# Kernel optimization log

Measured on AMD Instinct MI355X. Metric: run time of the kernel, lower is better.

The kernel has to match this reference:

```python
import jax, jax.numpy as jnp
import numpy as np

B, S, D, C = 4, 4096, 2048, 64  # batch, seq, d_model, num_channels (sqrt(4096)=64)
TEMP = 1.0
LN_EPS = 1e-5
AGG_EPS = 1e-8


def _layer_norm(x, g, b):
    m = x.mean(-1, keepdims=True)
    v = ((x - m) ** 2).mean(-1, keepdims=True)
    return (x - m) / jnp.sqrt(v + LN_EPS) * g + b


def setup_inputs() -> dict:
    key = jax.random.key(0)
    ks = jax.random.split(key, 8)
    s = 1.0 / np.sqrt(D)
    return {
        "x": jax.random.normal(ks[0], (B, S, D), jnp.float32),
        "attention_mask": jnp.ones((B, S), jnp.float32),
        "ln_gamma": jnp.ones((D,), jnp.float32),
        "ln_beta": jnp.zeros((D,), jnp.float32),
        "Wq": jax.random.normal(ks[1], (D, D), jnp.float32) * s,
        "Wk": jax.random.normal(ks[2], (D, D), jnp.float32) * s,
        "Wv": jax.random.normal(ks[3], (D, D), jnp.float32) * s,
        "Wr": jax.random.normal(ks[4], (C, D), jnp.float32) * s,
        "br": jnp.zeros((C,), jnp.float32),
        "Wa": jax.random.normal(ks[5], (D, D), jnp.float32) * s,
        "ba": jnp.zeros((D,), jnp.float32),
        "Wout": jax.random.normal(ks[6], (D, D), jnp.float32) * s,
        "bout": jnp.zeros((D,), jnp.float32),
    }


def reference(x, attention_mask, ln_gamma, ln_beta, Wq, Wk, Wv, Wr, br, Wa, ba, Wout, bout):
    residual = x
    h = _layer_norm(x, ln_gamma, ln_beta)
    q = h @ Wq.T  # [B,S,D]
    k = h @ Wk.T
    v = h @ Wv.T
    m = attention_mask[..., None]
    q = q * m
    k = k * m
    v = v * m

    # --- dynamic router: logits -> softmax, top-1 channel id + gathered weight ---
    routing_input = q + 0.1 * k
    probs = jax.nn.softmax((routing_input @ Wr.T + br) / TEMP, axis=-1)  # [B,S,C]
    channel_ids = jnp.argmax(probs, axis=-1)  # [B,S] int
    w = jnp.take_along_axis(probs, channel_ids[..., None], axis=-1)  # [B,S,1] top-1 weight

    # --- learnable channel aggregator: scatter-reduce tokens -> channels ---
    onehot = jax.nn.one_hot(channel_ids, C, dtype=v.dtype)  # [B,S,C]
    dispatch = onehot * w  # weighted dispatch mask
    ch_sum = jnp.einsum('bsc,bsd->bcd', dispatch, v)  # [B,C,D]
    ch_den = dispatch.sum(axis=1)  # [B,C]
    ch_mean = ch_sum / (ch_den[..., None] + AGG_EPS)
    ch_out = ch_mean @ Wa.T + ba  # learnable channel transform [B,C,D]
    # gather channel summary back to each token, weighted by routing weight
    aggregated = jnp.einsum('bsc,bcd->bsd', onehot, ch_out) * w  # [B,S,D]

    # --- regularization term ---
    q_norm = jnp.linalg.norm(q, axis=-1, keepdims=True)
    k_norm = jnp.linalg.norm(k, axis=-1, keepdims=True)
    reg = 0.001 * (q_norm + k_norm).mean()

    output = aggregated @ Wout.T + bout
    output = output + reg  # broadcast scalar reg_term
    output = output + residual
    return output
```

## Files before the change

### kernel.cpp

```cpp
#include <hip/hip_runtime.h>
#include <hip/hip_bf16.h>

typedef unsigned short u16;
typedef __bf16 bf16x8 __attribute__((ext_vector_type(8)));
typedef float  f32x4  __attribute__((ext_vector_type(4)));

#define B_   4
#define S_   4096
#define D_   2048
#define C_   64
#define T_   (B_*S_)
#define NALL 6144
#define NCH  16

__device__ __forceinline__ u16 f2bf(float f) {
  union { float f; unsigned u; } c; c.f = f;
  unsigned r = c.u + 0x7FFFu + ((c.u >> 16) & 1u);
  return (u16)(r >> 16);
}
__device__ __forceinline__ float bf2f(u16 u) {
  union { float f; unsigned u; } c; c.u = ((unsigned)u) << 16;
  return c.f;
}

__device__ __forceinline__ void gload16(const u16* g, u16* l) {
  __builtin_amdgcn_global_load_lds(
      (__attribute__((address_space(1))) void*)(void*)g,
      (__attribute__((address_space(3))) void*)l, 16, 0, 0);
}

template<int EPI>
__global__ __launch_bounds__(256)
void gemm_bt(const u16* __restrict__ A, const u16* __restrict__ BT, int K,
             const float* __restrict__ mask,
             float* __restrict__ qn2, float* __restrict__ kn2,
             u16* __restrict__ uout, float* __restrict__ fout,
             const float* __restrict__ bias)
{
  __shared__ u16 lA[128 * 32];
  __shared__ u16 lB[128 * 32];
  const int bm = blockIdx.x, bn = blockIdx.y;
  const int tid = threadIdx.x;
  const int wid = tid >> 6, lane = tid & 63;
  const int wm = wid >> 1, wn = wid & 1;
  const int lcol = lane & 15, khalf = lane >> 4;
  const int kb = khalf * 8;

  f32x4 acc[4][4] = {};

  const u16* Ab = A + (size_t)bm * 128 * K;
  const u16* Bb = BT + (size_t)bn * 128 * K;
  const int arow = wm * 64 + lcol;
  const int brow = wn * 64 + lcol;

  for (int kt = 0; kt < K; kt += 32) {
#pragma unroll
    for (int i = 0; i < 2; ++i) {
      int idx = tid + i * 256;
      int r = idx >> 2, ko = (idx & 3) << 3;
      gload16(Ab + (size_t)r * K + kt + ko, &lA[idx * 8]);
      gload16(Bb + (size_t)r * K + kt + ko, &lB[idx * 8]);
    }
    __syncthreads();
    bf16x8 av[4], bv[4];
#pragma unroll
    for (int f = 0; f < 4; ++f) {
      av[f] = *(const bf16x8*)&lA[(arow + f * 16) * 32 + kb];
      bv[f] = *(const bf16x8*)&lB[(brow + f * 16) * 32 + kb];
    }
#pragma unroll
    for (int m = 0; m < 4; ++m)
#pragma unroll
      for (int n = 0; n < 4; ++n)
        acc[m][n] = __builtin_amdgcn_mfma_f32_16x16x32_bf16(av[m], bv[n], acc[m][n], 0, 0, 0);
    __syncthreads();
  }

  const int r0 = bm * 128 + wm * 64;
  const int c0 = bn * 128 + wn * 64;
  const int lrow = khalf * 4;

  if constexpr (EPI == 0) {
    const int region = bn >> 4;
#pragma unroll
    for (int fm = 0; fm < 4; ++fm) {
#pragma unroll
      for (int i = 0; i < 4; ++i) {
        int row = r0 + fm * 16 + lrow + i;
        float mv = mask[row];
        if (region < 2) {
          float ss = 0.f;
#pragma unroll
          for (int fn = 0; fn < 4; ++fn) { float v = acc[fm][fn][i] * mv; ss += v * v; }
#pragma unroll
          for (int d = 1; d < 16; d <<= 1) ss += __shfl_xor(ss, d);
          if (lcol == 0) atomicAdd((region == 0 ? qn2 : kn2) + row, ss);
        } else {
#pragma unroll
          for (int fn = 0; fn < 4; ++fn) {
            int col = c0 + fn * 16 + lcol - 4096;
            uout[(size_t)row * D_ + col] = f2bf(acc[fm][fn][i] * mv);
          }
        }
      }
    }
  } else if constexpr (EPI == 2) {
#pragma unroll
    for (int fm = 0; fm < 4; ++fm)
#pragma unroll
      for (int i = 0; i < 4; ++i) {
        int row = r0 + fm * 16 + lrow + i;
#pragma unroll
        for (int fn = 0; fn < 4; ++fn) {
          int col = c0 + fn * 16 + lcol;
          uout[(size_t)row * D_ + col] = f2bf(acc[fm][fn][i] + bias[col]);
        }
      }
  } else {
#pragma unroll
    for (int fm = 0; fm < 4; ++fm)
#pragma unroll
      for (int i = 0; i < 4; ++i) {
        int row = r0 + fm * 16 + lrow + i;
#pragma unroll
        for (int fn = 0; fn < 4; ++fn) {
          int col = c0 + fn * 16 + lcol;
          fout[(size_t)row * D_ + col] = acc[fm][fn][i];
        }
      }
  }
}

__global__ __launch_bounds__(256)
void gemm4_bt(const u16* __restrict__ Ah, const u16* __restrict__ Al,
              const u16* __restrict__ Bh, const u16* __restrict__ Bl,
              int K, int rlim, float* __restrict__ out, int ldo)
{
  __shared__ u16 lAh[128 * 32];
  __shared__ u16 lAl[128 * 32];
  __shared__ u16 lBh[64 * 32];
  __shared__ u16 lBl[64 * 32];
  const int bm = blockIdx.x, bn = blockIdx.y;
  const int tid = threadIdx.x;
  const int wid = tid >> 6, lane = tid & 63;
  const int lcol = lane & 15, khalf = lane >> 4;
  const int kb = khalf * 8;

  f32x4 acc[2][4] = {};

  const u16* Abh = Ah + (size_t)bm * 128 * K;
  const u16* Abl = Al + (size_t)bm * 128 * K;
  const u16* Bbh = Bh + (size_t)bn * 64 * K;
  const u16* Bbl = Bl + (size_t)bn * 64 * K;
  const int arow = wid * 32 + lcol;

  for (int kt = 0; kt < K; kt += 32) {
#pragma unroll
    for (int i = 0; i < 2; ++i) {
      int idx = tid + i * 256;
      int r = idx >> 2, ko = (idx & 3) << 3;
      gload16(Abh + (size_t)r * K + kt + ko, &lAh[idx * 8]);
      gload16(Abl + (size_t)r * K + kt + ko, &lAl[idx * 8]);
    }
    {
      int r = tid >> 2, ko = (tid & 3) << 3;
      gload16(Bbh + (size_t)r * K + kt + ko, &lBh[tid * 8]);
      gload16(Bbl + (size_t)r * K + kt + ko, &lBl[tid * 8]);
    }
    __syncthreads();
    bf16x8 ah[2], al[2], bh[4], bl[4];
#pragma unroll
    for (int f = 0; f < 2; ++f) {
      ah[f] = *(const bf16x8*)&lAh[(arow + f * 16) * 32 + kb];
      al[f] = *(const bf16x8*)&lAl[(arow + f * 16) * 32 + kb];
    }
#pragma unroll
    for (int f = 0; f < 4; ++f) {
      bh[f] = *(const bf16x8*)&lBh[(f * 16 + lcol) * 32 + kb];
      bl[f] = *(const bf16x8*)&lBl[(f * 16 + lcol) * 32 + kb];
    }
#pragma unroll
    for (int m = 0; m < 2; ++m)
#pragma unroll
      for (int n = 0; n < 4; ++n) {
        acc[m][n] = __builtin_amdgcn_mfma_f32_16x16x32_bf16(ah[m], bh[n], acc[m][n], 0, 0, 0);
        acc[m][n] = __builtin_amdgcn_mfma_f32_16x16x32_bf16(ah[m], bl[n], acc[m][n], 0, 0, 0);
        acc[m][n] = __builtin_amdgcn_mfma_f32_16x16x32_bf16(al[m], bh[n], acc[m][n], 0, 0, 0);
        acc[m][n] = __builtin_amdgcn_mfma_f32_16x16x32_bf16(al[m], bl[n], acc[m][n], 0, 0, 0);
      }
    __syncthreads();
  }

  const int r0 = bm * 128 + wid * 32;
#pragma unroll
  for (int fm = 0; fm < 2; ++fm)
#pragma unroll
    for (int i = 0; i < 4; ++i) {
      int row = r0 + fm * 16 + khalf * 4 + i;
      if (row < rlim) {
#pragma unroll
        for (int fn = 0; fn < 4; ++fn) {
          int col = bn * 64 + fn * 16 + lcol;
          out[(size_t)row * ldo + col] = acc[fm][fn][i];
        }
      }
    }
}

__global__ __launch_bounds__(256)
void ln_kernel(const float* __restrict__ x, const float* __restrict__ g,
               const float* __restrict__ be, u16* __restrict__ h, u16* __restrict__ hl)
{
  const int row = blockIdx.x, tid = threadIdx.x;
  const int wid = tid >> 6, lane = tid & 63;
  const float* xr = x + (size_t)row * D_;
  float4 a = *(const float4*)(xr + tid * 4);
  float4 b = *(const float4*)(xr + 1024 + tid * 4);
  float s = a.x + a.y + a.z + a.w + b.x + b.y + b.z + b.w;
  float q = a.x * a.x + a.y * a.y + a.z * a.z + a.w * a.w +
            b.x * b.x + b.y * b.y + b.z * b.z + b.w * b.w;
#pragma unroll
  for (int d = 1; d < 64; d <<= 1) { s += __shfl_xor(s, d); q += __shfl_xor(q, d); }
  __shared__ float ls[4], lq[4];
  if (lane == 0) { ls[wid] = s; lq[wid] = q; }
  __syncthreads();
  s = ls[0] + ls[1] + ls[2] + ls[3];
  q = lq[0] + lq[1] + lq[2] + lq[3];
  const float mean = s * (1.0f / D_);
  const float var = q * (1.0f / D_) - mean * mean;
  const float rstd = rsqrtf(var + 1e-5f);

#pragma unroll
  for (int half = 0; half < 2; ++half) {
    int base = half * 1024 + tid * 4;
    float4 xv = half ? b : a;
    float4 gv = *(const float4*)(g + base);
    float4 bv = *(const float4*)(be + base);
    float v0 = (xv.x - mean) * rstd * gv.x + bv.x;
    float v1 = (xv.y - mean) * rstd * gv.y + bv.y;
    float v2 = (xv.z - mean) * rstd * gv.z + bv.z;
    float v3 = (xv.w - mean) * rstd * gv.w + bv.w;
    ushort4 oh, ol;
    oh.x = f2bf(v0); ol.x = f2bf(v0 - bf2f(oh.x));
    oh.y = f2bf(v1); ol.y = f2bf(v1 - bf2f(oh.y));
    oh.z = f2bf(v2); ol.z = f2bf(v2 - bf2f(oh.z));
    oh.w = f2bf(v3); ol.w = f2bf(v3 - bf2f(oh.w));
    *(ushort4*)(h  + (size_t)row * D_ + base) = oh;
    *(ushort4*)(hl + (size_t)row * D_ + base) = ol;
  }
}

__global__ __launch_bounds__(256)
void castf2b(const float* __restrict__ in, u16* __restrict__ out, int n)
{
  int i = (blockIdx.x * 256 + threadIdx.x) * 4;
  if (i >= n) return;
  float4 v = *(const float4*)(in + i);
  ushort4 o; o.x = f2bf(v.x); o.y = f2bf(v.y); o.z = f2bf(v.z); o.w = f2bf(v.w);
  *(ushort4*)(out + i) = o;
}

__global__ __launch_bounds__(256)
void splitf(const float* __restrict__ in, u16* __restrict__ hi, u16* __restrict__ lo, int n)
{
  int i = (blockIdx.x * 256 + threadIdx.x) * 4;
  if (i >= n) return;
  float4 v = *(const float4*)(in + i);
  ushort4 h, l;
  h.x = f2bf(v.x); l.x = f2bf(v.x - bf2f(h.x));
  h.y = f2bf(v.y); l.y = f2bf(v.y - bf2f(h.y));
  h.z = f2bf(v.z); l.z = f2bf(v.z - bf2f(h.z));
  h.w = f2bf(v.w); l.w = f2bf(v.w - bf2f(h.w));
  *(ushort4*)(hi + i) = h;
  *(ushort4*)(lo + i) = l;
}

__global__ __launch_bounds__(256)
void wqk_t(const float* __restrict__ Wq, const float* __restrict__ Wk,
           u16* __restrict__ Th, u16* __restrict__ Tl)
{
  __shared__ float t[32][33];
  const int bx = blockIdx.x * 32, by = blockIdx.y * 32;
  const int tx = threadIdx.x & 31, ty = threadIdx.x >> 5;
#pragma unroll
  for (int j = 0; j < 32; j += 8) {
    int aa = by + ty + j, ee = bx + tx;
    t[ty + j][tx] = Wq[(size_t)aa * D_ + ee] + 0.1f * Wk[(size_t)aa * D_ + ee];
  }
  __syncthreads();
#pragma unroll
  for (int j = 0; j < 32; j += 8) {
    int ee = bx + ty + j, aa = by + tx;
    float v = t[tx][ty + j];
    u16 h = f2bf(v);
    Th[(size_t)ee * D_ + aa] = h;
    Tl[(size_t)ee * D_ + aa] = f2bf(v - bf2f(h));
  }
}

__global__ __launch_bounds__(256)
void reg_reduce(const float* __restrict__ qn2, const float* __restrict__ kn2,
                float* __restrict__ racc)
{
  int i = blockIdx.x * 256 + threadIdx.x;
  int lane = threadIdx.x & 63, wid = threadIdx.x >> 6;
  float v = sqrtf(qn2[i]) + sqrtf(kn2[i]);
#pragma unroll
  for (int d = 1; d < 64; d <<= 1) v += __shfl_xor(v, d);
  __shared__ float lsum[4];
  if (lane == 0) lsum[wid] = v;
  __syncthreads();
  if (threadIdx.x == 0) atomicAdd(racc, lsum[0] + lsum[1] + lsum[2] + lsum[3]);
}

__global__ __launch_bounds__(256)
void router_kernel(const float* __restrict__ logits, const float* __restrict__ br,
                   int* __restrict__ cid, float* __restrict__ wt, float* __restrict__ chden)
{
  const int tid = threadIdx.x, wid = tid >> 6, lane = tid & 63;
  const int t = blockIdx.x * 4 + wid;
  float l = logits[(size_t)t * C_ + lane] + br[lane];
  float mx = l;
#pragma unroll
  for (int d = 1; d < 64; d <<= 1) mx = fmaxf(mx, __shfl_xor(mx, d));
  float e = __expf(l - mx);
  float s = e;
#pragma unroll
  for (int d = 1; d < 64; d <<= 1) s += __shfl_xor(s, d);
  unsigned long long ball = __ballot(l == mx);
  if (lane == 0) {
    int cstar = __ffsll(ball) - 1;
    float ww = 1.0f / s;
    cid[t] = cstar;
    wt[t] = ww;
    atomicAdd(&chden[(t >> 12) * C_ + cstar], ww);
  }
}

__global__ __launch_bounds__(256)
void scatter_kernel(const u16* __restrict__ v, const int* __restrict__ cid,
                    const float* __restrict__ w, float* __restrict__ partial)
{
  __shared__ float acc[C_ * 256];
  const int b = blockIdx.x, dt = blockIdx.y, st = blockIdx.z;
  const int tid = threadIdx.x;
  for (int i = tid; i < C_ * 256; i += 256) acc[i] = 0.f;
  __syncthreads();
  const int d = dt * 256 + tid;
  const int tbase = b * S_ + st * (S_ / NCH);
  for (int s = 0; s < S_ / NCH; ++s) {
    int t = tbase + s;
    int c = cid[t];
    float ww = w[t];
    acc[c * 256 + tid] += ww * bf2f(v[(size_t)t * D_ + d]);
  }
  __syncthreads();
  float* pb = partial + ((size_t)(b * NCH + st) * C_) * D_ + dt * 256;
  for (int i = tid; i < C_ * 256; i += 256) {
    int c = i >> 8, dd = i & 255;
    pb[(size_t)c * D_ + dd] = acc[i];
  }
}

__global__ __launch_bounds__(256)
void chmean_kernel(const float* __restrict__ partial, const float* __restrict__ chden,
                   u16* __restrict__ chmean)
{
  int idx = blockIdx.x * 256 + threadIdx.x;
  int d = idx & 2047, c = (idx >> 11) & 63, b = idx >> 17;
  float ssum = 0.f;
#pragma unroll
  for (int st = 0; st < NCH; ++st)
    ssum += partial[((size_t)(b * NCH + st) * C_ + c) * D_ + d];
  float den = chden[b * C_ + c];
  chmean[idx] = f2bf(ssum / (den + 1e-8f));
}

__global__ __launch_bounds__(256)
void finalize_kernel(const float* __restrict__ x, const float* __restrict__ bout,
                     const float* __restrict__ chproj, const int* __restrict__ cid,
                     const float* __restrict__ wt, const float* __restrict__ racc,
                     float* __restrict__ out)
{
  const int row = blockIdx.x, tid = threadIdx.x;
  const int b = row >> 12;
  const int c = cid[row];
  const float ww = wt[row];
  const float reg = racc[0] * (0.001f / (float)T_);
  const float* cp = chproj + (size_t)(b * C_ + c) * D_;
  const float* xr = x + (size_t)row * D_;
  float* orow = out + (size_t)row * D_;
#pragma unroll
  for (int base = 0; base < D_; base += 1024) {
    int d = base + tid * 4;
    float4 xv = *(const float4*)(xr + d);
    float4 cv = *(const float4*)(cp + d);
    float4 bv = *(const float4*)(bout + d);
    float4 o;
    o.x = ww * cv.x + bv.x + reg + xv.x;
    o.y = ww * cv.y + bv.y + reg + xv.y;
    o.z = ww * cv.z + bv.z + reg + xv.z;
    o.w = ww * cv.w + bv.w + reg + xv.w;
    *(float4*)(orow + d) = o;
  }
}

extern "C" void kernel_launch(void* const* d_in, const int* in_sizes, int n_in,
                              void* d_out, int out_size, void* d_ws, size_t ws_size,
                              hipStream_t stream)
{
  const float* x     = (const float*)d_in[0];
  const float* mask  = (const float*)d_in[1];
  const float* gamma = (const float*)d_in[2];
  const float* beta  = (const float*)d_in[3];
  const float* Wq    = (const float*)d_in[4];
  const float* Wk    = (const float*)d_in[5];
  const float* Wv    = (const float*)d_in[6];
  const float* Wr    = (const float*)d_in[7];
  const float* br    = (const float*)d_in[8];
  const float* Wa    = (const float*)d_in[9];
  const float* ba    = (const float*)d_in[10];
  const float* Wout  = (const float*)d_in[11];
  const float* bout  = (const float*)d_in[12];
  float* out = (float*)d_out;

  char* p = (char*)d_ws;
  size_t off = 0;
  auto take = [&](size_t bytes) -> void* {
    void* r = p + off;
    off = (off + bytes + 255) & ~(size_t)255;
    return r;
  };

  u16*   Wall   = (u16*)take((size_t)NALL * D_ * 2);
  u16*   WrPh   = (u16*)take((size_t)128 * D_ * 2);
  u16*   WrPl   = (u16*)take((size_t)128 * D_ * 2);
  u16*   Wqkh   = (u16*)take((size_t)D_ * D_ * 2);
  u16*   Wqkl   = (u16*)take((size_t)D_ * D_ * 2);
  u16*   WaB    = (u16*)take((size_t)D_ * D_ * 2);
  u16*   WoutB  = (u16*)take((size_t)D_ * D_ * 2);
  u16*   hbuf   = (u16*)take((size_t)T_ * D_ * 2);
  u16*   hlbuf  = (u16*)take((size_t)T_ * D_ * 2);
  u16*   vbuf   = (u16*)take((size_t)T_ * D_ * 2);
  float* Mf     = (float*)take((size_t)C_ * D_ * 4);
  u16*   Mh     = (u16*)take((size_t)C_ * D_ * 2);
  u16*   Ml     = (u16*)take((size_t)C_ * D_ * 2);
  float* logits = (float*)take((size_t)T_ * C_ * 4);
  float* partial= (float*)take((size_t)B_ * NCH * C_ * D_ * 4);
  float* chproj = (float*)take((size_t)B_ * C_ * D_ * 4);
  u16*   chmean = (u16*)take((size_t)B_ * C_ * D_ * 2);
  u16*   choutb = (u16*)take((size_t)B_ * C_ * D_ * 2);
  int*   cid    = (int*)take((size_t)T_ * 4);
  float* wt     = (float*)take((size_t)T_ * 4);
  char*  zbeg   = p + off;
  float* qn2    = (float*)take((size_t)T_ * 4);
  float* kn2    = (float*)take((size_t)T_ * 4);
  float* chden  = (float*)take((size_t)B_ * C_ * 4);
  float* racc   = (float*)take(256);
  size_t zlen   = (size_t)((p + off) - zbeg);

  hipMemsetAsync(zbeg, 0, zlen, stream);
  hipMemsetAsync(WrPh + (size_t)C_ * D_, 0, (size_t)C_ * D_ * 2, stream);
  hipMemsetAsync(WrPl + (size_t)C_ * D_, 0, (size_t)C_ * D_ * 2, stream);

  const int cb = 256;
  castf2b<<<dim3((D_ * D_) / 1024), cb, 0, stream>>>(Wq, Wall, D_ * D_);
  castf2b<<<dim3((D_ * D_) / 1024), cb, 0, stream>>>(Wk, Wall + (size_t)D_ * D_, D_ * D_);
  castf2b<<<dim3((D_ * D_) / 1024), cb, 0, stream>>>(Wv, Wall + (size_t)2 * D_ * D_, D_ * D_);
  castf2b<<<dim3((D_ * D_) / 1024), cb, 0, stream>>>(Wa, WaB, D_ * D_);
  castf2b<<<dim3((D_ * D_) / 1024), cb, 0, stream>>>(Wout, WoutB, D_ * D_);
  splitf<<<dim3((C_ * D_) / 1024), cb, 0, stream>>>(Wr, WrPh, WrPl, C_ * D_);
  wqk_t<<<dim3(64, 64), cb, 0, stream>>>(Wq, Wk, Wqkh, Wqkl);
  ln_kernel<<<dim3(T_), cb, 0, stream>>>(x, gamma, beta, hbuf, hlbuf);

  gemm4_bt<<<dim3(1, D_ / 64), cb, 0, stream>>>(WrPh, WrPl, Wqkh, Wqkl, D_, C_, Mf, D_);
  splitf<<<dim3((C_ * D_) / 1024), cb, 0, stream>>>(Mf, Mh, Ml, C_ * D_);
  gemm4_bt<<<dim3(T_ / 128, 1), cb, 0, stream>>>(hbuf, hlbuf, Mh, Ml, D_, T_, logits, C_);

  gemm_bt<0><<<dim3(T_ / 128, NALL / 128), cb, 0, stream>>>(hbuf, Wall, D_, mask, qn2, kn2,
                                                            vbuf, nullptr, nullptr);
  reg_reduce<<<dim3(T_ / 256), cb, 0, stream>>>(qn2, kn2, racc);
  router_kernel<<<dim3(T_ / 4), cb, 0, stream>>>(logits, br, cid, wt, chden);
  scatter_kernel<<<dim3(B_, D_ / 256, NCH), cb, 0, stream>>>(vbuf, cid, wt, partial);
  chmean_kernel<<<dim3((B_ * C_ * D_) / 256), cb, 0, stream>>>(partial, chden, chmean);
  gemm_bt<2><<<dim3(2, 16), cb, 0, stream>>>(chmean, WaB, D_, nullptr, nullptr, nullptr,
                                             choutb, nullptr, ba);
  gemm_bt<3><<<dim3(2, 16), cb, 0, stream>>>(choutb, WoutB, D_, nullptr, nullptr, nullptr,
                                             nullptr, chproj, nullptr);
  finalize_kernel<<<dim3(T_), cb, 0, stream>>>(x, bout, chproj, cid, wt, racc, out);
}
```

Baseline: 1.284 ms.

## Replace QKV GEMM with 256x256 double-buffered 8-wave kernel and swizzle LDS

Replaces the 128x128 single-buffered QKV projection GEMM with a new 256x256-tile kernel using 512 threads and 128KB of dynamic LDS. It double-buffers in LDS, interleaves global-to-LDS staging with MFMA phases under explicit barriers and vmcnt waits, and uses XOR-swizzled LDS layouts. The aim is more data reuse per tile, overlap of loads with compute, and fewer LDS bank conflicts in the dominant GEMM. The remaining small GEMMs also get an XOR swizzle on their LDS chunks. The hand-scheduled barrier and wait sequence is fragile, and the larger LDS footprint limits occupancy.

```diff
diff --git a/kernel.cpp b/kernel.cpp
--- a/kernel.cpp
+++ b/kernel.cpp
@@ -29,11 +29,164 @@
       (__attribute__((address_space(3))) void*)l, 16, 0, 0);
 }
 
+#define BAR()  { __builtin_amdgcn_s_barrier(); __builtin_amdgcn_sched_barrier(0); }
+#define VMW(N) { asm volatile("s_waitcnt vmcnt(" #N ")" ::: "memory"); __builtin_amdgcn_sched_barrier(0); }
+
+template<int REGB, int TYPE>
+__device__ __forceinline__ void stage_ht(const u16* __restrict__ Mat, char* lds,
+                                         int bufbyte, int kelem, int wid, int lane)
+{
+#pragma unroll
+  for (int j = 0; j < 2; ++j) {
+    int sr;
+    if (TYPE == 0)      sr = (j ?  64 :   0) + wid * 8;
+    else if (TYPE == 1) sr = (j ? 192 : 128) + wid * 8;
+    else if (TYPE == 2) sr = (j ? 128 :   0) + wid * 8;
+    else                sr = (j ? 192 :  64) + wid * 8;
+    int r  = sr + (lane >> 3);
+    int kc = (lane & 7) ^ (lane >> 3);
+    const u16* src = Mat + (size_t)r * 2048 + kelem + kc * 8;
+    u16* dst = (u16*)(lds + bufbyte + REGB * 32768 + sr * 128 + lane * 16);
+    gload16(src, dst);
+  }
+}
+
+__global__ __launch_bounds__(512, 2)
+void qkv8(const u16* __restrict__ A, const u16* __restrict__ BT,
+          const float* __restrict__ mask,
+          float* __restrict__ qn2, float* __restrict__ kn2,
+          u16* __restrict__ vout)
+{
+  extern __shared__ char lds[];
+  const int tid = threadIdx.x;
+  const int wid = tid >> 6, lane = tid & 63;
+  const int wm = wid >> 2, wn = wid & 3;
+  const int lcol = lane & 15, lhi = lane >> 4, lc7 = lane & 7;
+  const int bm = blockIdx.x, bn = blockIdx.y;
+
+  const u16* Ab_ = A  + (size_t)bm * 256 * 2048;
+  const u16* Bb_ = BT + (size_t)bn * 256 * 2048;
+
+  f32x4 acc[8][4] = {};
+  bf16x8 afr[4][2], bfr[4][2];
+
+#define LDA_(f_, s_) (*(const bf16x8*)(lds + cbyte + ((wm*128 + (f_)*16 + lcol) * 128) + (((lhi + (s_)*4) ^ lc7) << 4)))
+#define LDB_(g_, s_) (*(const bf16x8*)(lds + cbyte + 32768 + ((wn*64 + (g_)*16 + lcol) * 128) + (((lhi + (s_)*4) ^ lc7) << 4)))
+
+  stage_ht<1, 0>(Bb_, lds, 0, 0, wid, lane);
+  stage_ht<1, 1>(Bb_, lds, 0, 0, wid, lane);
+  stage_ht<0, 2>(Ab_, lds, 0, 0, wid, lane);
+  stage_ht<0, 3>(Ab_, lds, 0, 0, wid, lane);
+  VMW(2); BAR();
+
+#pragma unroll 2
+  for (int kt = 0; kt < 32; ++kt) {
+    const int cbyte = (kt & 1) * 65536;
+    const int nbyte = cbyte ^ 65536;
+    const int kel = ((kt + 1) & 31) * 64;
+
+#pragma unroll
+    for (int g = 0; g < 4; ++g)
+#pragma unroll
+      for (int s = 0; s < 2; ++s) bfr[g][s] = LDB_(g, s);
+#pragma unroll
+    for (int f = 0; f < 4; ++f)
+#pragma unroll
+      for (int s = 0; s < 2; ++s) afr[f][s] = LDA_(f, s);
+    stage_ht<1, 0>(Bb_, lds, nbyte, kel, wid, lane);
+    BAR();
+    __builtin_amdgcn_s_setprio(1);
+#pragma unroll
+    for (int f = 0; f < 4; ++f)
+#pragma unroll
+      for (int g = 0; g < 2; ++g)
+#pragma unroll
+        for (int s = 0; s < 2; ++s)
+          acc[f][g] = __builtin_amdgcn_mfma_f32_16x16x32_bf16(afr[f][s], bfr[g][s], acc[f][g], 0, 0, 0);
+    __builtin_amdgcn_s_setprio(0);
+    BAR();
+
+    stage_ht<1, 1>(Bb_, lds, nbyte, kel, wid, lane);
+    BAR();
+    __builtin_amdgcn_s_setprio(1);
+#pragma unroll
+    for (int f = 0; f < 4; ++f)
+#pragma unroll
+      for (int g = 2; g < 4; ++g)
+#pragma unroll
+        for (int s = 0; s < 2; ++s)
+          acc[f][g] = __builtin_amdgcn_mfma_f32_16x16x32_bf16(afr[f][s], bfr[g][s], acc[f][g], 0, 0, 0);
+    __builtin_amdgcn_s_setprio(0);
+    VMW(4); BAR();
+
+#pragma unroll
+    for (int f = 0; f < 4; ++f)
+#pragma unroll
+      for (int s = 0; s < 2; ++s) afr[f][s] = LDA_(f + 4, s);
+    stage_ht<0, 2>(Ab_, lds, nbyte, kel, wid, lane);
+    BAR();
+    __builtin_amdgcn_s_setprio(1);
+#pragma unroll
+    for (int f = 0; f < 4; ++f)
+#pragma unroll
+      for (int g = 0; g < 2; ++g)
+#pragma unroll
+        for (int s = 0; s < 2; ++s)
+          acc[f + 4][g] = __builtin_amdgcn_mfma_f32_16x16x32_bf16(afr[f][s], bfr[g][s], acc[f + 4][g], 0, 0, 0);
+    __builtin_amdgcn_s_setprio(0);
+    BAR();
+
+    stage_ht<0, 3>(Ab_, lds, nbyte, kel, wid, lane);
+    BAR();
+    __builtin_amdgcn_s_setprio(1);
+#pragma unroll
+    for (int f = 0; f < 4; ++f)
+#pragma unroll
+      for (int g = 2; g < 4; ++g)
+#pragma unroll
+        for (int s = 0; s < 2; ++s)
+          acc[f + 4][g] = __builtin_amdgcn_mfma_f32_16x16x32_bf16(afr[f][s], bfr[g][s], acc[f + 4][g], 0, 0, 0);
+    __builtin_amdgcn_s_setprio(0);
+    VMW(2); BAR();
+  }
+#undef LDA_
+#undef LDB_
+
+  const int region = bn >> 3;
+  const int grow0 = bm * 256 + wm * 128;
+  if (region < 2) {
+    float* dst = region ? kn2 : qn2;
+#pragma unroll
+    for (int f = 0; f < 8; ++f)
+#pragma unroll
+      for (int i = 0; i < 4; ++i) {
+        int row = grow0 + f * 16 + lhi * 4 + i;
+        float mv = mask[row];
+        float ss = 0.f;
+#pragma unroll
+        for (int g = 0; g < 4; ++g) { float v = acc[f][g][i] * mv; ss += v * v; }
+#pragma unroll
+        for (int d = 1; d < 16; d <<= 1) ss += __shfl_xor(ss, d);
+        if (lcol == 0) atomicAdd(dst + row, ss);
+      }
+  } else {
+    const int gcol0 = (bn - 16) * 256 + wn * 64 + lcol;
+#pragma unroll
+    for (int f = 0; f < 8; ++f)
+#pragma unroll
+      for (int i = 0; i < 4; ++i) {
+        int row = grow0 + f * 16 + lhi * 4 + i;
+        float mv = mask[row];
+#pragma unroll
+        for (int g = 0; g < 4; ++g)
+          vout[(size_t)row * D_ + gcol0 + g * 16] = f2bf(acc[f][g][i] * mv);
+      }
+  }
+}
+
 template<int EPI>
 __global__ __launch_bounds__(256)
 void gemm_bt(const u16* __restrict__ A, const u16* __restrict__ BT, int K,
-             const float* __restrict__ mask,
-             float* __restrict__ qn2, float* __restrict__ kn2,
              u16* __restrict__ uout, float* __restrict__ fout,
              const float* __restrict__ bias)
 {
@@ -44,7 +197,8 @@
   const int wid = tid >> 6, lane = tid & 63;
   const int wm = wid >> 1, wn = wid & 1;
   const int lcol = lane & 15, khalf = lane >> 4;
-  const int kb = khalf * 8;
+  const int csw = khalf ^ ((lcol >> 1) & 3);
+  const int kb = csw * 8;
 
   f32x4 acc[4][4] = {};
 
@@ -57,7 +211,9 @@
 #pragma unroll
     for (int i = 0; i < 2; ++i) {
       int idx = tid + i * 256;
-      int r = idx >> 2, ko = (idx & 3) << 3;
+      int r = idx >> 2;
+      int kc = (idx & 3) ^ ((r >> 1) & 3);
+      int ko = kc << 3;
       gload16(Ab + (size_t)r * K + kt + ko, &lA[idx * 8]);
       gload16(Bb + (size_t)r * K + kt + ko, &lB[idx * 8]);
     }
@@ -80,31 +236,7 @@
   const int c0 = bn * 128 + wn * 64;
   const int lrow = khalf * 4;
 
-  if constexpr (EPI == 0) {
-    const int region = bn >> 4;
-#pragma unroll
-    for (int fm = 0; fm < 4; ++fm) {
-#pragma unroll
-      for (int i = 0; i < 4; ++i) {
-        int row = r0 + fm * 16 + lrow + i;
-        float mv = mask[row];
-        if (region < 2) {
-          float ss = 0.f;
-#pragma unroll
-          for (int fn = 0; fn < 4; ++fn) { float v = acc[fm][fn][i] * mv; ss += v * v; }
-#pragma unroll
-          for (int d = 1; d < 16; d <<= 1) ss += __shfl_xor(ss, d);
-          if (lcol == 0) atomicAdd((region == 0 ? qn2 : kn2) + row, ss);
-        } else {
-#pragma unroll
-          for (int fn = 0; fn < 4; ++fn) {
-            int col = c0 + fn * 16 + lcol - 4096;
-            uout[(size_t)row * D_ + col] = f2bf(acc[fm][fn][i] * mv);
-          }
-        }
-      }
-    }
-  } else if constexpr (EPI == 2) {
+  if constexpr (EPI == 2) {
 #pragma unroll
     for (int fm = 0; fm < 4; ++fm)
 #pragma unroll
@@ -144,7 +276,8 @@
   const int tid = threadIdx.x;
   const int wid = tid >> 6, lane = tid & 63;
   const int lcol = lane & 15, khalf = lane >> 4;
-  const int kb = khalf * 8;
+  const int csw = khalf ^ ((lcol >> 1) & 3);
+  const int kb = csw * 8;
 
   f32x4 acc[2][4] = {};
 
@@ -158,12 +291,16 @@
 #pragma unroll
     for (int i = 0; i < 2; ++i) {
       int idx = tid + i * 256;
-      int r = idx >> 2, ko = (idx & 3) << 3;
+      int r = idx >> 2;
+      int kc = (idx & 3) ^ ((r >> 1) & 3);
+      int ko = kc << 3;
       gload16(Abh + (size_t)r * K + kt + ko, &lAh[idx * 8]);
       gload16(Abl + (size_t)r * K + kt + ko, &lAl[idx * 8]);
     }
     {
-      int r = tid >> 2, ko = (tid & 3) << 3;
+      int r = tid >> 2;
+      int kc = (tid & 3) ^ ((r >> 1) & 3);
+      int ko = kc << 3;
       gload16(Bbh + (size_t)r * K + kt + ko, &lBh[tid * 8]);
       gload16(Bbl + (size_t)r * K + kt + ko, &lBl[tid * 8]);
     }
@@ -477,15 +614,14 @@
   splitf<<<dim3((C_ * D_) / 1024), cb, 0, stream>>>(Mf, Mh, Ml, C_ * D_);
   gemm4_bt<<<dim3(T_ / 128, 1), cb, 0, stream>>>(hbuf, hlbuf, Mh, Ml, D_, T_, logits, C_);
 
-  gemm_bt<0><<<dim3(T_ / 128, NALL / 128), cb, 0, stream>>>(hbuf, Wall, D_, mask, qn2, kn2,
-                                                            vbuf, nullptr, nullptr);
+  hipFuncSetAttribute((const void*)qkv8, hipFuncAttributeMaxDynamicSharedMemorySize, 131072);
+  qkv8<<<dim3(T_ / 256, NALL / 256), 512, 131072, stream>>>(hbuf, Wall, mask, qn2, kn2, vbuf);
+
   reg_reduce<<<dim3(T_ / 256), cb, 0, stream>>>(qn2, kn2, racc);
   router_kernel<<<dim3(T_ / 4), cb, 0, stream>>>(logits, br, cid, wt, chden);
   scatter_kernel<<<dim3(B_, D_ / 256, NCH), cb, 0, stream>>>(vbuf, cid, wt, partial);
   chmean_kernel<<<dim3((B_ * C_ * D_) / 256), cb, 0, stream>>>(partial, chden, chmean);
-  gemm_bt<2><<<dim3(2, 16), cb, 0, stream>>>(chmean, WaB, D_, nullptr, nullptr, nullptr,
-                                             choutb, nullptr, ba);
-  gemm_bt<3><<<dim3(2, 16), cb, 0, stream>>>(choutb, WoutB, D_, nullptr, nullptr, nullptr,
-                                             nullptr, chproj, nullptr);
+  gemm_bt<2><<<dim3(2, 16), cb, 0, stream>>>(chmean, WaB, D_, choutb, nullptr, ba);
+  gemm_bt<3><<<dim3(2, 16), cb, 0, stream>>>(choutb, WoutB, D_, nullptr, chproj, nullptr);
   finalize_kernel<<<dim3(T_), cb, 0, stream>>>(x, bout, chproj, cid, wt, racc, out);
 }
```

Measured after the change: 1.078 ms. 16.1% less time.
